# Optimization experiments

Hardware: AMD Instinct MI355X
Metric: run time of the kernel (lower is better)

The kernel has to match this reference:

```python
import jax, jax.numpy as jnp
import numpy as np

B, D, K = 131072, 64, 4096

def setup_inputs() -> dict:
    key = jax.random.key(0)
    k1, k2 = jax.random.split(key)
    z_e = jax.random.normal(k1, (B, D), dtype=jnp.float32)
    # nn.init.uniform_(-1/K, 1/K)
    codebook = jax.random.uniform(k2, (K, D), dtype=jnp.float32, minval=-1.0 / K, maxval=1.0 / K)
    return {"z_e": z_e, "codebook": codebook}

def reference(z_e, codebook):
    # squared-distance expansion: ||z||^2 + ||e||^2 - 2 z.e  -> (B, K)
    z2 = jnp.sum(z_e * z_e, axis=1, keepdims=True)          # (B, 1)
    e2 = jnp.sum(codebook * codebook, axis=1)[None, :]       # (1, K)
    ze = jnp.einsum('bd,kd->bk', z_e, codebook)              # (B, K)
    dist = z2 + e2 - 2.0 * ze
    codes = jnp.argmin(dist, axis=1)                         # (B,) int
    z_q = codebook[codes]                                    # (B, D) gather
    return (z_q, codes)
```

## Files before the change

### kernel.cpp

```cpp
#include <hip/hip_runtime.h>
#include <math.h>
#include <stdint.h>

#define Bn 131072
#define Dn 64
#define Kn 4096
#define TK 64
#define NKT (Kn / TK)

typedef _Float16 f16x8 __attribute__((ext_vector_type(8)));
typedef float f32x4 __attribute__((ext_vector_type(4)));

__device__ __forceinline__ unsigned umn(unsigned a, unsigned b) { return a < b ? a : b; }
__device__ __forceinline__ unsigned umx(unsigned a, unsigned b) { return a > b ? a : b; }
__device__ __forceinline__ unsigned umed3(unsigned a, unsigned b, unsigned c) {
  unsigned d;
  asm("v_med3_u32 %0, %1, %2, %3" : "=v"(d) : "v"(a), "v"(b), "v"(c));
  return d;
}
__device__ __forceinline__ unsigned umn3(unsigned a, unsigned b, unsigned c) {
  return umn(umn(a, b), c);
}

__device__ __forceinline__ void stage16(const void* g, void* l) {
  __builtin_amdgcn_global_load_lds((const __attribute__((address_space(1))) unsigned int*)g,
                                   (__attribute__((address_space(3))) unsigned int*)l,
                                   16, 0, 0);
}

__global__ __launch_bounds__(256) void cvt_cb(const float* __restrict__ cb,
                                              unsigned char* __restrict__ img) {
  int u = blockIdx.x * 256 + threadIdx.x;
  int g = u >> 3;
  int p = u & 7;
  int kt = g >> 6;
  int n = g & 63;
  const float4* s = (const float4*)(cb + (size_t)g * Dn + p * 8);
  float4 c0 = s[0], c1 = s[1];
  f16x8 h;
  h[0] = (_Float16)(c0.x * 4096.f); h[1] = (_Float16)(c0.y * 4096.f);
  h[2] = (_Float16)(c0.z * 4096.f); h[3] = (_Float16)(c0.w * 4096.f);
  h[4] = (_Float16)(c1.x * 4096.f); h[5] = (_Float16)(c1.y * 4096.f);
  h[6] = (_Float16)(c1.z * 4096.f); h[7] = (_Float16)(c1.w * 4096.f);
  *(f16x8*)(img + (size_t)kt * 8192 + n * 128 + ((p ^ (n & 7)) << 4)) = h;
}

__global__ __launch_bounds__(512, 4) void vq_main(const float* __restrict__ z,
                                                  const float* __restrict__ cb,
                                                  const unsigned char* __restrict__ img,
                                                  float* __restrict__ out) {
  __shared__ __align__(16) unsigned char smem[34816];
  unsigned char* tb0 = smem;
  unsigned char* tb1 = smem + 8192;
  const int tid = threadIdx.x;
  const int lane = tid & 63;
  const int w = tid >> 6;
  const int q = lane >> 4;
  const int col = lane & 15;
  const int row0 = blockIdx.x * 256;

  const unsigned char* wsrc = img + tid * 16;
  stage16(wsrc, tb0 + tid * 16);

  f16x8 A[2][2];
#pragma unroll
  for (int i = 0; i < 2; ++i)
#pragma unroll
    for (int c = 0; c < 2; ++c) {
      const float* zp = z + (size_t)(row0 + w * 32 + i * 16 + col) * Dn + c * 32 + q * 8;
      float4 x0 = *(const float4*)zp;
      float4 x1 = *(const float4*)(zp + 4);
      f16x8 a;
      a[0] = (_Float16)(-2.f * x0.x); a[1] = (_Float16)(-2.f * x0.y);
      a[2] = (_Float16)(-2.f * x0.z); a[3] = (_Float16)(-2.f * x0.w);
      a[4] = (_Float16)(-2.f * x1.x); a[5] = (_Float16)(-2.f * x1.y);
      a[6] = (_Float16)(-2.f * x1.z); a[7] = (_Float16)(-2.f * x1.w);
      A[i][c] = a;
    }

  f32x4 acc[2][4];
  unsigned k1[2][4], k2[2][4];
#pragma unroll
  for (int i = 0; i < 2; ++i)
#pragma unroll
    for (int r = 0; r < 4; ++r) { k1[i][r] = 0xFFFFFFFFu; k2[i][r] = 0xFFFFFFFFu; }
  unsigned tg[4] = {0u, 1u, 2u, 3u};
  const f32x4 c256 = {256.f, 256.f, 256.f, 256.f};

  for (int kt = 0; kt < NKT; ++kt) {
    unsigned char* tcur = (kt & 1) ? tb1 : tb0;
    unsigned char* tnxt = (kt & 1) ? tb0 : tb1;
    if (kt + 1 < NKT) {
      stage16(wsrc + (size_t)(kt + 1) * 8192, tnxt + tid * 16);
      asm volatile("s_waitcnt vmcnt(1)" ::: "memory");
    } else {
      asm volatile("s_waitcnt vmcnt(0)" ::: "memory");
    }
    __builtin_amdgcn_s_barrier();
    __builtin_amdgcn_sched_barrier(0);

#pragma unroll
    for (int c = 0; c < 2; ++c)
#pragma unroll
      for (int t = 0; t < 4; ++t) {
        f16x8 Bf = *(const f16x8*)(tcur + (t * 16 + col) * 128 + (((c * 4 + q) ^ (col & 7)) << 4));
#pragma unroll
        for (int i = 0; i < 2; ++i)
          acc[i][t] = __builtin_amdgcn_mfma_f32_16x16x32_f16(A[i][c], Bf,
                                                             (c == 0) ? c256 : acc[i][t], 0, 0, 0);
      }

#pragma unroll
    for (int i = 0; i < 2; ++i)
#pragma unroll
      for (int r = 0; r < 4; ++r) {
        unsigned K0 = (__float_as_uint(acc[i][0][r]) & 0xFFFFFF00u) | tg[0];
        unsigned K1v = (__float_as_uint(acc[i][1][r]) & 0xFFFFFF00u) | tg[1];
        unsigned K2v = (__float_as_uint(acc[i][2][r]) & 0xFFFFFF00u) | tg[2];
        unsigned K3v = (__float_as_uint(acc[i][3][r]) & 0xFFFFFF00u) | tg[3];
        unsigned s1 = umn(K0, K1v), s2 = umx(K0, K1v);
        unsigned s3 = umn(K2v, K3v), s4 = umx(K2v, K3v);
        unsigned m3 = umed3(k1[i][r], s1, s3);
        unsigned n3 = umn3(k2[i][r], s2, s4);
        k1[i][r] = umn3(k1[i][r], s1, s3);
        k2[i][r] = umn(m3, n3);
      }
#pragma unroll
    for (int t = 0; t < 4; ++t) tg[t] += 4;

    __builtin_amdgcn_s_barrier();
  }

  __syncthreads();
  unsigned* dmp = (unsigned*)smem;
#pragma unroll
  for (int i = 0; i < 2; ++i)
#pragma unroll
    for (int r = 0; r < 4; ++r) {
      int rr = i * 16 + q * 4 + r;
      int rb = w * 32 + rr;
      dmp[rb * 33 + col * 2] = k1[i][r];
      dmp[rb * 33 + col * 2 + 1] = k2[i][r];
    }
  __syncthreads();

  {
    const int rl = tid >> 1;
    const int half = tid & 1;
    const unsigned* keys = dmp + rl * 33 + half * 16;
    unsigned mk = 0xFFFFFFFFu;
    for (int j = 0; j < 16; ++j) mk = umn(mk, keys[j]);
    const float lim = __uint_as_float(mk & 0xFFFFFF00u) + 0.5f;

    const float4* zr4 = (const float4*)(z + (size_t)(row0 + rl) * Dn);

    float r8[8];
#pragma unroll
    for (int g = 0; g < 2; ++g) {
      float4 v = zr4[g]; int j = g * 4;
      r8[j + 0] = __fmul_rn(v.x, v.x); r8[j + 1] = __fmul_rn(v.y, v.y);
      r8[j + 2] = __fmul_rn(v.z, v.z); r8[j + 3] = __fmul_rn(v.w, v.w);
    }
#pragma unroll
    for (int g = 2; g < 16; ++g) {
      float4 v = zr4[g]; int j = (g & 1) * 4;
      r8[j + 0] = __fadd_rn(r8[j + 0], __fmul_rn(v.x, v.x));
      r8[j + 1] = __fadd_rn(r8[j + 1], __fmul_rn(v.y, v.y));
      r8[j + 2] = __fadd_rn(r8[j + 2], __fmul_rn(v.z, v.z));
      r8[j + 3] = __fadd_rn(r8[j + 3], __fmul_rn(v.w, v.w));
    }
    float z2f = __fadd_rn(__fadd_rn(__fadd_rn(r8[0], r8[1]), __fadd_rn(r8[2], r8[3])),
                          __fadd_rn(__fadd_rn(r8[4], r8[5]), __fadd_rn(r8[6], r8[7])));

    float bq = INFINITY; int bc = Kn;
    for (int j = 0; j < 16; ++j) {
      unsigned key = keys[j];
      float sc = __uint_as_float(key & 0xFFFFFF00u);
      if (sc > lim) continue;
      int cnd = half * 16 + j;
      int tag = (int)(key & 0xFFu);
      int code = (tag >> 2) * 64 + (tag & 3) * 16 + (cnd >> 1);
      const float4* cr = (const float4*)(cb + (size_t)code * Dn);
      double ze = 0.0;
      float e8[8];
#pragma unroll
      for (int g = 0; g < 16; ++g) {
        float4 ev = cr[g]; float4 zv = zr4[g];
        ze += (double)ev.x * (double)zv.x + (double)ev.y * (double)zv.y +
              (double)ev.z * (double)zv.z + (double)ev.w * (double)zv.w;
        int jj = (g & 1) * 4;
        if (g < 2) {
          e8[jj + 0] = __fmul_rn(ev.x, ev.x); e8[jj + 1] = __fmul_rn(ev.y, ev.y);
          e8[jj + 2] = __fmul_rn(ev.z, ev.z); e8[jj + 3] = __fmul_rn(ev.w, ev.w);
        } else {
          e8[jj + 0] = __fadd_rn(e8[jj + 0], __fmul_rn(ev.x, ev.x));
          e8[jj + 1] = __fadd_rn(e8[jj + 1], __fmul_rn(ev.y, ev.y));
          e8[jj + 2] = __fadd_rn(e8[jj + 2], __fmul_rn(ev.z, ev.z));
          e8[jj + 3] = __fadd_rn(e8[jj + 3], __fmul_rn(ev.w, ev.w));
        }
      }
      float e2f = __fadd_rn(__fadd_rn(__fadd_rn(e8[0], e8[1]), __fadd_rn(e8[2], e8[3])),
                            __fadd_rn(__fadd_rn(e8[4], e8[5]), __fadd_rn(e8[6], e8[7])));
      float zef = (float)ze;
      float t1 = __fadd_rn(z2f, e2f);
      float t2 = __fmul_rn(2.0f, zef);
      float qv = __fadd_rn(t1, -t2);
      if (qv < bq || (qv == bq && code < bc)) { bq = qv; bc = code; }
    }
    float obq = __shfl_xor(bq, 1);
    int obc = __shfl_xor(bc, 1);
    if (obq < bq || (obq == bq && obc < bc)) { bq = obq; bc = obc; }
    if (half == 0) {
      ((int*)(smem + 33792))[rl] = bc;
      out[(size_t)Bn * Dn + row0 + rl] = (float)bc;
    }
  }
  __syncthreads();

  {
    const float4* cb4 = (const float4*)cb;
    float4* out4 = (float4*)out;
    const int* wc = (const int*)(smem + 33792);
#pragma unroll
    for (int i = 0; i < 8; ++i) {
      int t = i * 512 + tid;
      int r = t >> 4, c2 = t & 15;
      int wn = wc[r];
      out4[(size_t)(row0 + r) * 16 + c2] = cb4[(size_t)wn * 16 + c2];
    }
  }
}

extern "C" void kernel_launch(void* const* d_in, const int* in_sizes, int n_in,
                              void* d_out, int out_size, void* d_ws, size_t ws_size,
                              hipStream_t stream) {
  const float* z = (const float*)d_in[0];
  const float* cb = (const float*)d_in[1];
  float* out = (float*)d_out;
  unsigned char* img = (unsigned char*)d_ws;
  cvt_cb<<<128, 256, 0, stream>>>(cb, img);
  vq_main<<<Bn / 256, 512, 0, stream>>>(z, cb, img, out);
}
```

Before: 193.0 us.

## Halve rows per block to one 16-row MFMA tile per wave, raise occupancy

Each wave now handles 16 rows instead of 32, so a block covers 128 rows and the grid doubles. This frees registers and LDS so launch bounds go from 4 to 8 blocks per SM, and the refinement phase is split across four threads per row with a two-step shuffle reduction. The tag encoding changes so that 64 tiles fit in 8 bits. The cost is that each staged codebook tile is reused by half as many rows, which doubles codebook LDS traffic and barrier work per output row.

```diff
diff --git a/kernel.cpp b/kernel.cpp
--- a/kernel.cpp
+++ b/kernel.cpp
@@ -7,6 +7,7 @@
 #define Kn 4096
 #define TK 64
 #define NKT (Kn / TK)
+#define RPB 128
 
 typedef _Float16 f16x8 __attribute__((ext_vector_type(8)));
 typedef float f32x4 __attribute__((ext_vector_type(4)));
@@ -45,11 +46,11 @@
   *(f16x8*)(img + (size_t)kt * 8192 + n * 128 + ((p ^ (n & 7)) << 4)) = h;
 }
 
-__global__ __launch_bounds__(512, 4) void vq_main(const float* __restrict__ z,
+__global__ __launch_bounds__(512, 8) void vq_main(const float* __restrict__ z,
                                                   const float* __restrict__ cb,
                                                   const unsigned char* __restrict__ img,
                                                   float* __restrict__ out) {
-  __shared__ __align__(16) unsigned char smem[34816];
+  __shared__ __align__(16) unsigned char smem[17408];
   unsigned char* tb0 = smem;
   unsigned char* tb1 = smem + 8192;
   const int tid = threadIdx.x;
@@ -57,34 +58,30 @@
   const int w = tid >> 6;
   const int q = lane >> 4;
   const int col = lane & 15;
-  const int row0 = blockIdx.x * 256;
+  const int row0 = blockIdx.x * RPB;
 
   const unsigned char* wsrc = img + tid * 16;
   stage16(wsrc, tb0 + tid * 16);
 
-  f16x8 A[2][2];
-#pragma unroll
-  for (int i = 0; i < 2; ++i)
-#pragma unroll
-    for (int c = 0; c < 2; ++c) {
-      const float* zp = z + (size_t)(row0 + w * 32 + i * 16 + col) * Dn + c * 32 + q * 8;
-      float4 x0 = *(const float4*)zp;
-      float4 x1 = *(const float4*)(zp + 4);
-      f16x8 a;
-      a[0] = (_Float16)(-2.f * x0.x); a[1] = (_Float16)(-2.f * x0.y);
-      a[2] = (_Float16)(-2.f * x0.z); a[3] = (_Float16)(-2.f * x0.w);
-      a[4] = (_Float16)(-2.f * x1.x); a[5] = (_Float16)(-2.f * x1.y);
-      a[6] = (_Float16)(-2.f * x1.z); a[7] = (_Float16)(-2.f * x1.w);
-      A[i][c] = a;
-    }
-
-  f32x4 acc[2][4];
-  unsigned k1[2][4], k2[2][4];
-#pragma unroll
-  for (int i = 0; i < 2; ++i)
-#pragma unroll
-    for (int r = 0; r < 4; ++r) { k1[i][r] = 0xFFFFFFFFu; k2[i][r] = 0xFFFFFFFFu; }
-  unsigned tg[4] = {0u, 1u, 2u, 3u};
+  f16x8 A[2];
+#pragma unroll
+  for (int c = 0; c < 2; ++c) {
+    const float* zp = z + (size_t)(row0 + w * 16 + col) * Dn + c * 32 + q * 8;
+    float4 x0 = *(const float4*)zp;
+    float4 x1 = *(const float4*)(zp + 4);
+    f16x8 a;
+    a[0] = (_Float16)(-2.f * x0.x); a[1] = (_Float16)(-2.f * x0.y);
+    a[2] = (_Float16)(-2.f * x0.z); a[3] = (_Float16)(-2.f * x0.w);
+    a[4] = (_Float16)(-2.f * x1.x); a[5] = (_Float16)(-2.f * x1.y);
+    a[6] = (_Float16)(-2.f * x1.z); a[7] = (_Float16)(-2.f * x1.w);
+    A[c] = a;
+  }
+
+  f32x4 acc[4];
+  unsigned k1[4], k2[4];
+#pragma unroll
+  for (int r = 0; r < 4; ++r) { k1[r] = 0xFFFFFFFFu; k2[r] = 0xFFFFFFFFu; }
+  unsigned tg[4] = {0u << 6, 1u << 6, 2u << 6, 3u << 6};
   const f32x4 c256 = {256.f, 256.f, 256.f, 256.f};
 
   for (int kt = 0; kt < NKT; ++kt) {
@@ -104,29 +101,25 @@
 #pragma unroll
       for (int t = 0; t < 4; ++t) {
         f16x8 Bf = *(const f16x8*)(tcur + (t * 16 + col) * 128 + (((c * 4 + q) ^ (col & 7)) << 4));
-#pragma unroll
-        for (int i = 0; i < 2; ++i)
-          acc[i][t] = __builtin_amdgcn_mfma_f32_16x16x32_f16(A[i][c], Bf,
-                                                             (c == 0) ? c256 : acc[i][t], 0, 0, 0);
+        acc[t] = __builtin_amdgcn_mfma_f32_16x16x32_f16(A[c], Bf,
+                                                        (c == 0) ? c256 : acc[t], 0, 0, 0);
       }
 
 #pragma unroll
-    for (int i = 0; i < 2; ++i)
-#pragma unroll
-      for (int r = 0; r < 4; ++r) {
-        unsigned K0 = (__float_as_uint(acc[i][0][r]) & 0xFFFFFF00u) | tg[0];
-        unsigned K1v = (__float_as_uint(acc[i][1][r]) & 0xFFFFFF00u) | tg[1];
-        unsigned K2v = (__float_as_uint(acc[i][2][r]) & 0xFFFFFF00u) | tg[2];
-        unsigned K3v = (__float_as_uint(acc[i][3][r]) & 0xFFFFFF00u) | tg[3];
-        unsigned s1 = umn(K0, K1v), s2 = umx(K0, K1v);
-        unsigned s3 = umn(K2v, K3v), s4 = umx(K2v, K3v);
-        unsigned m3 = umed3(k1[i][r], s1, s3);
-        unsigned n3 = umn3(k2[i][r], s2, s4);
-        k1[i][r] = umn3(k1[i][r], s1, s3);
-        k2[i][r] = umn(m3, n3);
-      }
-#pragma unroll
-    for (int t = 0; t < 4; ++t) tg[t] += 4;
+    for (int r = 0; r < 4; ++r) {
+      unsigned K0 = (__float_as_uint(acc[0][r]) & 0xFFFFFF00u) | tg[0];
+      unsigned K1v = (__float_as_uint(acc[1][r]) & 0xFFFFFF00u) | tg[1];
+      unsigned K2v = (__float_as_uint(acc[2][r]) & 0xFFFFFF00u) | tg[2];
+      unsigned K3v = (__float_as_uint(acc[3][r]) & 0xFFFFFF00u) | tg[3];
+      unsigned s1 = umn(K0, K1v), s2 = umx(K0, K1v);
+      unsigned s3 = umn(K2v, K3v), s4 = umx(K2v, K3v);
+      unsigned m3 = umed3(k1[r], s1, s3);
+      unsigned n3 = umn3(k2[r], s2, s4);
+      k1[r] = umn3(k1[r], s1, s3);
+      k2[r] = umn(m3, n3);
+    }
+#pragma unroll
+    for (int t = 0; t < 4; ++t) tg[t] += 1;
 
     __builtin_amdgcn_s_barrier();
   }
@@ -134,22 +127,19 @@
   __syncthreads();
   unsigned* dmp = (unsigned*)smem;
 #pragma unroll
-  for (int i = 0; i < 2; ++i)
-#pragma unroll
-    for (int r = 0; r < 4; ++r) {
-      int rr = i * 16 + q * 4 + r;
-      int rb = w * 32 + rr;
-      dmp[rb * 33 + col * 2] = k1[i][r];
-      dmp[rb * 33 + col * 2 + 1] = k2[i][r];
-    }
+  for (int r = 0; r < 4; ++r) {
+    int rb = w * 16 + q * 4 + r;
+    dmp[rb * 33 + col * 2] = k1[r];
+    dmp[rb * 33 + col * 2 + 1] = k2[r];
+  }
   __syncthreads();
 
   {
-    const int rl = tid >> 1;
-    const int half = tid & 1;
-    const unsigned* keys = dmp + rl * 33 + half * 16;
+    const int rl = tid >> 2;
+    const int qt = tid & 3;
+    const unsigned* keys = dmp + rl * 33 + qt * 8;
     unsigned mk = 0xFFFFFFFFu;
-    for (int j = 0; j < 16; ++j) mk = umn(mk, keys[j]);
+    for (int j = 0; j < 8; ++j) mk = umn(mk, keys[j]);
     const float lim = __uint_as_float(mk & 0xFFFFFF00u) + 0.5f;
 
     const float4* zr4 = (const float4*)(z + (size_t)(row0 + rl) * Dn);
@@ -173,13 +163,13 @@
                           __fadd_rn(__fadd_rn(r8[4], r8[5]), __fadd_rn(r8[6], r8[7])));
 
     float bq = INFINITY; int bc = Kn;
-    for (int j = 0; j < 16; ++j) {
+    for (int j = 0; j < 8; ++j) {
       unsigned key = keys[j];
       float sc = __uint_as_float(key & 0xFFFFFF00u);
       if (sc > lim) continue;
-      int cnd = half * 16 + j;
+      int c2 = qt * 8 + j;
       int tag = (int)(key & 0xFFu);
-      int code = (tag >> 2) * 64 + (tag & 3) * 16 + (cnd >> 1);
+      int code = (tag & 63) * 64 + (tag >> 6) * 16 + (c2 >> 1);
       const float4* cr = (const float4*)(cb + (size_t)code * Dn);
       double ze = 0.0;
       float e8[8];
@@ -207,11 +197,14 @@
       float qv = __fadd_rn(t1, -t2);
       if (qv < bq || (qv == bq && code < bc)) { bq = qv; bc = code; }
     }
-    float obq = __shfl_xor(bq, 1);
-    int obc = __shfl_xor(bc, 1);
-    if (obq < bq || (obq == bq && obc < bc)) { bq = obq; bc = obc; }
-    if (half == 0) {
-      ((int*)(smem + 33792))[rl] = bc;
+#pragma unroll
+    for (int d = 1; d <= 2; d <<= 1) {
+      float obq = __shfl_xor(bq, d);
+      int obc = __shfl_xor(bc, d);
+      if (obq < bq || (obq == bq && obc < bc)) { bq = obq; bc = obc; }
+    }
+    if (qt == 0) {
+      ((int*)(smem + 16896))[rl] = bc;
       out[(size_t)Bn * Dn + row0 + rl] = (float)bc;
     }
   }
@@ -220,9 +213,9 @@
   {
     const float4* cb4 = (const float4*)cb;
     float4* out4 = (float4*)out;
-    const int* wc = (const int*)(smem + 33792);
-#pragma unroll
-    for (int i = 0; i < 8; ++i) {
+    const int* wc = (const int*)(smem + 16896);
+#pragma unroll
+    for (int i = 0; i < 4; ++i) {
       int t = i * 512 + tid;
       int r = t >> 4, c2 = t & 15;
       int wn = wc[r];
@@ -239,5 +232,5 @@
   float* out = (float*)d_out;
   unsigned char* img = (unsigned char*)d_ws;
   cvt_cb<<<128, 256, 0, stream>>>(cb, img);
-  vq_main<<<Bn / 256, 512, 0, stream>>>(z, cb, img, out);
-}
+  vq_main<<<Bn / RPB, 512, 0, stream>>>(z, cb, img, out);
+}
```

After: 255.6 us. +32.4%, slower.

## Load codebook fragments directly from global memory instead of LDS staging

Applied to the files above, without the earlier changes.

Removes the double-buffered global-to-LDS staging of codebook tiles and the per-tile barriers; each lane now reads its fp16 B fragments directly from a row-major global image, relying on cache hits. Block size is halved to 256 threads covering 128 rows, and the candidate tag encoding is changed to match the new layout. This trades barrier and LDS traffic for redundant per-wave global/L1 reads of the codebook.

```diff
diff --git a/kernel.cpp b/kernel.cpp
--- a/kernel.cpp
+++ b/kernel.cpp
@@ -7,6 +7,7 @@
 #define Kn 4096
 #define TK 64
 #define NKT (Kn / TK)
+#define RPB 128
 
 typedef _Float16 f16x8 __attribute__((ext_vector_type(8)));
 typedef float f32x4 __attribute__((ext_vector_type(4)));
@@ -22,45 +23,30 @@
   return umn(umn(a, b), c);
 }
 
-__device__ __forceinline__ void stage16(const void* g, void* l) {
-  __builtin_amdgcn_global_load_lds((const __attribute__((address_space(1))) unsigned int*)g,
-                                   (__attribute__((address_space(3))) unsigned int*)l,
-                                   16, 0, 0);
-}
-
 __global__ __launch_bounds__(256) void cvt_cb(const float* __restrict__ cb,
                                               unsigned char* __restrict__ img) {
   int u = blockIdx.x * 256 + threadIdx.x;
-  int g = u >> 3;
-  int p = u & 7;
-  int kt = g >> 6;
-  int n = g & 63;
-  const float4* s = (const float4*)(cb + (size_t)g * Dn + p * 8);
+  const float4* s = (const float4*)(cb + (size_t)u * 8);
   float4 c0 = s[0], c1 = s[1];
   f16x8 h;
   h[0] = (_Float16)(c0.x * 4096.f); h[1] = (_Float16)(c0.y * 4096.f);
   h[2] = (_Float16)(c0.z * 4096.f); h[3] = (_Float16)(c0.w * 4096.f);
   h[4] = (_Float16)(c1.x * 4096.f); h[5] = (_Float16)(c1.y * 4096.f);
   h[6] = (_Float16)(c1.z * 4096.f); h[7] = (_Float16)(c1.w * 4096.f);
-  *(f16x8*)(img + (size_t)kt * 8192 + n * 128 + ((p ^ (n & 7)) << 4)) = h;
-}
-
-__global__ __launch_bounds__(512, 4) void vq_main(const float* __restrict__ z,
+  ((f16x8*)img)[u] = h;
+}
+
+__global__ __launch_bounds__(256, 4) void vq_main(const float* __restrict__ z,
                                                   const float* __restrict__ cb,
                                                   const unsigned char* __restrict__ img,
                                                   float* __restrict__ out) {
-  __shared__ __align__(16) unsigned char smem[34816];
-  unsigned char* tb0 = smem;
-  unsigned char* tb1 = smem + 8192;
+  __shared__ __align__(16) unsigned char smem[17408];
   const int tid = threadIdx.x;
   const int lane = tid & 63;
   const int w = tid >> 6;
   const int q = lane >> 4;
   const int col = lane & 15;
-  const int row0 = blockIdx.x * 256;
-
-  const unsigned char* wsrc = img + tid * 16;
-  stage16(wsrc, tb0 + tid * 16);
+  const int row0 = blockIdx.x * RPB;
 
   f16x8 A[2][2];
 #pragma unroll
@@ -84,31 +70,27 @@
   for (int i = 0; i < 2; ++i)
 #pragma unroll
     for (int r = 0; r < 4; ++r) { k1[i][r] = 0xFFFFFFFFu; k2[i][r] = 0xFFFFFFFFu; }
-  unsigned tg[4] = {0u, 1u, 2u, 3u};
+  unsigned tg[4] = {0u << 6, 1u << 6, 2u << 6, 3u << 6};
   const f32x4 c256 = {256.f, 256.f, 256.f, 256.f};
 
+  const f16x8* bp = (const f16x8*)img + col * 8 + q;
+
   for (int kt = 0; kt < NKT; ++kt) {
-    unsigned char* tcur = (kt & 1) ? tb1 : tb0;
-    unsigned char* tnxt = (kt & 1) ? tb0 : tb1;
-    if (kt + 1 < NKT) {
-      stage16(wsrc + (size_t)(kt + 1) * 8192, tnxt + tid * 16);
-      asm volatile("s_waitcnt vmcnt(1)" ::: "memory");
-    } else {
-      asm volatile("s_waitcnt vmcnt(0)" ::: "memory");
-    }
-    __builtin_amdgcn_s_barrier();
-    __builtin_amdgcn_sched_barrier(0);
-
+    f16x8 Bf[2][4];
 #pragma unroll
     for (int c = 0; c < 2; ++c)
 #pragma unroll
-      for (int t = 0; t < 4; ++t) {
-        f16x8 Bf = *(const f16x8*)(tcur + (t * 16 + col) * 128 + (((c * 4 + q) ^ (col & 7)) << 4));
+      for (int t = 0; t < 4; ++t)
+        Bf[c][t] = bp[kt * 512 + t * 128 + c * 4];
+
+#pragma unroll
+    for (int c = 0; c < 2; ++c)
+#pragma unroll
+      for (int t = 0; t < 4; ++t)
 #pragma unroll
         for (int i = 0; i < 2; ++i)
-          acc[i][t] = __builtin_amdgcn_mfma_f32_16x16x32_f16(A[i][c], Bf,
+          acc[i][t] = __builtin_amdgcn_mfma_f32_16x16x32_f16(A[i][c], Bf[c][t],
                                                              (c == 0) ? c256 : acc[i][t], 0, 0, 0);
-      }
 
 #pragma unroll
     for (int i = 0; i < 2; ++i)
@@ -126,19 +108,15 @@
         k2[i][r] = umn(m3, n3);
       }
 #pragma unroll
-    for (int t = 0; t < 4; ++t) tg[t] += 4;
-
-    __builtin_amdgcn_s_barrier();
+    for (int t = 0; t < 4; ++t) tg[t] += 1;
   }
 
-  __syncthreads();
   unsigned* dmp = (unsigned*)smem;
 #pragma unroll
   for (int i = 0; i < 2; ++i)
 #pragma unroll
     for (int r = 0; r < 4; ++r) {
-      int rr = i * 16 + q * 4 + r;
-      int rb = w * 32 + rr;
+      int rb = w * 32 + i * 16 + q * 4 + r;
       dmp[rb * 33 + col * 2] = k1[i][r];
       dmp[rb * 33 + col * 2 + 1] = k2[i][r];
     }
@@ -177,9 +155,9 @@
       unsigned key = keys[j];
       float sc = __uint_as_float(key & 0xFFFFFF00u);
       if (sc > lim) continue;
-      int cnd = half * 16 + j;
+      int c2 = half * 16 + j;
       int tag = (int)(key & 0xFFu);
-      int code = (tag >> 2) * 64 + (tag & 3) * 16 + (cnd >> 1);
+      int code = (tag & 63) * 64 + (tag >> 6) * 16 + (c2 >> 1);
       const float4* cr = (const float4*)(cb + (size_t)code * Dn);
       double ze = 0.0;
       float e8[8];
@@ -211,7 +189,7 @@
     int obc = __shfl_xor(bc, 1);
     if (obq < bq || (obq == bq && obc < bc)) { bq = obq; bc = obc; }
     if (half == 0) {
-      ((int*)(smem + 33792))[rl] = bc;
+      ((int*)(smem + 16896))[rl] = bc;
       out[(size_t)Bn * Dn + row0 + rl] = (float)bc;
     }
   }
@@ -220,10 +198,10 @@
   {
     const float4* cb4 = (const float4*)cb;
     float4* out4 = (float4*)out;
-    const int* wc = (const int*)(smem + 33792);
+    const int* wc = (const int*)(smem + 16896);
 #pragma unroll
     for (int i = 0; i < 8; ++i) {
-      int t = i * 512 + tid;
+      int t = i * 256 + tid;
       int r = t >> 4, c2 = t & 15;
       int wn = wc[r];
       out4[(size_t)(row0 + r) * 16 + c2] = cb4[(size_t)wn * 16 + c2];
@@ -239,5 +217,5 @@
   float* out = (float*)d_out;
   unsigned char* img = (unsigned char*)d_ws;
   cvt_cb<<<128, 256, 0, stream>>>(cb, img);
-  vq_main<<<Bn / 256, 512, 0, stream>>>(z, cb, img, out);
-}
+  vq_main<<<Bn / RPB, 256, 0, stream>>>(z, cb, img, out);
+}
```

After: 351.8 us. 82.3% more time.

## Stage four codebook tiles per round to cut barriers in the distance loop

Applied to the files above, without the earlier changes.

The main loop now loads four 64-code tiles into a 32 KB LDS buffer per round, double-buffered across rounds, in place of one 8 KB tile per iteration. This cuts the per-tile waitcnt and the two barriers down to one wait and one barrier per four tiles. The candidate tag encoding is reworked to hold the tile index in the low six bits and the column group above it, and the code decoding is changed to match. Total LDS rises to about 65 KB, so fewer blocks fit on each CU than the launch bounds ask for, which risks losing latency hiding.

```diff
diff --git a/kernel.cpp b/kernel.cpp
--- a/kernel.cpp
+++ b/kernel.cpp
@@ -7,6 +7,8 @@
 #define Kn 4096
 #define TK 64
 #define NKT (Kn / TK)
+#define TPR 4
+#define NRD (NKT / TPR)
 
 typedef _Float16 f16x8 __attribute__((ext_vector_type(8)));
 typedef float f32x4 __attribute__((ext_vector_type(4)));
@@ -49,9 +51,9 @@
                                                   const float* __restrict__ cb,
                                                   const unsigned char* __restrict__ img,
                                                   float* __restrict__ out) {
-  __shared__ __align__(16) unsigned char smem[34816];
-  unsigned char* tb0 = smem;
-  unsigned char* tb1 = smem + 8192;
+  __shared__ __align__(16) unsigned char smem[66560];
+  unsigned char* bufA = smem;
+  unsigned char* bufB = smem + 32768;
   const int tid = threadIdx.x;
   const int lane = tid & 63;
   const int w = tid >> 6;
@@ -60,7 +62,9 @@
   const int row0 = blockIdx.x * 256;
 
   const unsigned char* wsrc = img + tid * 16;
-  stage16(wsrc, tb0 + tid * 16);
+#pragma unroll
+  for (int j = 0; j < TPR; ++j)
+    stage16(wsrc + (size_t)j * 8192, bufA + j * 8192 + tid * 16);
 
   f16x8 A[2][2];
 #pragma unroll
@@ -84,51 +88,53 @@
   for (int i = 0; i < 2; ++i)
 #pragma unroll
     for (int r = 0; r < 4; ++r) { k1[i][r] = 0xFFFFFFFFu; k2[i][r] = 0xFFFFFFFFu; }
-  unsigned tg[4] = {0u, 1u, 2u, 3u};
+  unsigned tg[4] = {0u << 6, 1u << 6, 2u << 6, 3u << 6};
   const f32x4 c256 = {256.f, 256.f, 256.f, 256.f};
 
-  for (int kt = 0; kt < NKT; ++kt) {
-    unsigned char* tcur = (kt & 1) ? tb1 : tb0;
-    unsigned char* tnxt = (kt & 1) ? tb0 : tb1;
-    if (kt + 1 < NKT) {
-      stage16(wsrc + (size_t)(kt + 1) * 8192, tnxt + tid * 16);
-      asm volatile("s_waitcnt vmcnt(1)" ::: "memory");
-    } else {
-      asm volatile("s_waitcnt vmcnt(0)" ::: "memory");
-    }
+  for (int rd = 0; rd < NRD; ++rd) {
+    unsigned char* bcur = (rd & 1) ? bufB : bufA;
+    unsigned char* bnxt = (rd & 1) ? bufA : bufB;
+    asm volatile("s_waitcnt vmcnt(0)" ::: "memory");
     __builtin_amdgcn_s_barrier();
     __builtin_amdgcn_sched_barrier(0);
-
-#pragma unroll
-    for (int c = 0; c < 2; ++c)
-#pragma unroll
-      for (int t = 0; t < 4; ++t) {
-        f16x8 Bf = *(const f16x8*)(tcur + (t * 16 + col) * 128 + (((c * 4 + q) ^ (col & 7)) << 4));
-#pragma unroll
-        for (int i = 0; i < 2; ++i)
-          acc[i][t] = __builtin_amdgcn_mfma_f32_16x16x32_f16(A[i][c], Bf,
-                                                             (c == 0) ? c256 : acc[i][t], 0, 0, 0);
-      }
-
-#pragma unroll
-    for (int i = 0; i < 2; ++i)
-#pragma unroll
-      for (int r = 0; r < 4; ++r) {
-        unsigned K0 = (__float_as_uint(acc[i][0][r]) & 0xFFFFFF00u) | tg[0];
-        unsigned K1v = (__float_as_uint(acc[i][1][r]) & 0xFFFFFF00u) | tg[1];
-        unsigned K2v = (__float_as_uint(acc[i][2][r]) & 0xFFFFFF00u) | tg[2];
-        unsigned K3v = (__float_as_uint(acc[i][3][r]) & 0xFFFFFF00u) | tg[3];
-        unsigned s1 = umn(K0, K1v), s2 = umx(K0, K1v);
-        unsigned s3 = umn(K2v, K3v), s4 = umx(K2v, K3v);
-        unsigned m3 = umed3(k1[i][r], s1, s3);
-        unsigned n3 = umn3(k2[i][r], s2, s4);
-        k1[i][r] = umn3(k1[i][r], s1, s3);
-        k2[i][r] = umn(m3, n3);
-      }
-#pragma unroll
-    for (int t = 0; t < 4; ++t) tg[t] += 4;
-
-    __builtin_amdgcn_s_barrier();
+    if (rd + 1 < NRD) {
+#pragma unroll
+      for (int j = 0; j < TPR; ++j)
+        stage16(wsrc + ((size_t)(rd + 1) * TPR + j) * 8192, bnxt + j * 8192 + tid * 16);
+    }
+
+#pragma unroll
+    for (int j = 0; j < TPR; ++j) {
+      const unsigned char* tb = bcur + j * 8192;
+#pragma unroll
+      for (int c = 0; c < 2; ++c)
+#pragma unroll
+        for (int t = 0; t < 4; ++t) {
+          f16x8 Bf = *(const f16x8*)(tb + (t * 16 + col) * 128 + (((c * 4 + q) ^ (col & 7)) << 4));
+#pragma unroll
+          for (int i = 0; i < 2; ++i)
+            acc[i][t] = __builtin_amdgcn_mfma_f32_16x16x32_f16(A[i][c], Bf,
+                                                               (c == 0) ? c256 : acc[i][t], 0, 0, 0);
+        }
+
+#pragma unroll
+      for (int i = 0; i < 2; ++i)
+#pragma unroll
+        for (int r = 0; r < 4; ++r) {
+          unsigned K0 = (__float_as_uint(acc[i][0][r]) & 0xFFFFFF00u) | tg[0];
+          unsigned K1v = (__float_as_uint(acc[i][1][r]) & 0xFFFFFF00u) | tg[1];
+          unsigned K2v = (__float_as_uint(acc[i][2][r]) & 0xFFFFFF00u) | tg[2];
+          unsigned K3v = (__float_as_uint(acc[i][3][r]) & 0xFFFFFF00u) | tg[3];
+          unsigned s1 = umn(K0, K1v), s2 = umx(K0, K1v);
+          unsigned s3 = umn(K2v, K3v), s4 = umx(K2v, K3v);
+          unsigned m3 = umed3(k1[i][r], s1, s3);
+          unsigned n3 = umn3(k2[i][r], s2, s4);
+          k1[i][r] = umn3(k1[i][r], s1, s3);
+          k2[i][r] = umn(m3, n3);
+        }
+#pragma unroll
+      for (int t = 0; t < 4; ++t) tg[t] += 1;
+    }
   }
 
   __syncthreads();
@@ -137,8 +143,7 @@
   for (int i = 0; i < 2; ++i)
 #pragma unroll
     for (int r = 0; r < 4; ++r) {
-      int rr = i * 16 + q * 4 + r;
-      int rb = w * 32 + rr;
+      int rb = w * 32 + i * 16 + q * 4 + r;
       dmp[rb * 33 + col * 2] = k1[i][r];
       dmp[rb * 33 + col * 2 + 1] = k2[i][r];
     }
@@ -177,9 +182,9 @@
       unsigned key = keys[j];
       float sc = __uint_as_float(key & 0xFFFFFF00u);
       if (sc > lim) continue;
-      int cnd = half * 16 + j;
+      int c2 = half * 16 + j;
       int tag = (int)(key & 0xFFu);
-      int code = (tag >> 2) * 64 + (tag & 3) * 16 + (cnd >> 1);
+      int code = (tag & 63) * 64 + (tag >> 6) * 16 + (c2 >> 1);
       const float4* cr = (const float4*)(cb + (size_t)code * Dn);
       double ze = 0.0;
       float e8[8];
@@ -211,7 +216,7 @@
     int obc = __shfl_xor(bc, 1);
     if (obq < bq || (obq == bq && obc < bc)) { bq = obq; bc = obc; }
     if (half == 0) {
-      ((int*)(smem + 33792))[rl] = bc;
+      ((int*)(smem + 65536))[rl] = bc;
       out[(size_t)Bn * Dn + row0 + rl] = (float)bc;
     }
   }
@@ -220,7 +225,7 @@
   {
     const float4* cb4 = (const float4*)cb;
     float4* out4 = (float4*)out;
-    const int* wc = (const int*)(smem + 33792);
+    const int* wc = (const int*)(smem + 65536);
 #pragma unroll
     for (int i = 0; i < 8; ++i) {
       int t = i * 512 + tid;
```

Result: slower. 205.4 us (+6.4%).
